# Performance work log

Measured on AMD Instinct MI355X. Metric: run time of the kernel, lower is better.

## Reference

```python
import jax, jax.numpy as jnp
import numpy as np

E, K_TOP, NC = 8, 2, 5
B, L = 64, 512
BN_EPS = 1e-5


def conv1d(x, w, b, pad):
    # x: [B,C,L], w: [O,I,K] (torch OIH layout)
    y = jax.lax.conv_general_dilated(x, w, window_strides=(1,), padding=[(pad, pad)],
                                     dimension_numbers=('NCH', 'OIH', 'NCH'))
    return y + b[None, :, None]


def bn_eval(x, g, b, m, v):
    return g[None, :, None] * (x - m[None, :, None]) * jax.lax.rsqrt(v[None, :, None] + BN_EPS) + b[None, :, None]


def maxpool2(x):
    b, c, l = x.shape
    return x.reshape(b, c, l // 2, 2).max(-1)


def setup_inputs() -> dict:
    key = jax.random.key(0)
    ks = iter(jax.random.split(key, 80))
    nrm = lambda shape, s=0.05: jax.random.normal(next(ks), shape, jnp.float32) * s
    uni = lambda shape: jax.random.uniform(next(ks), shape, jnp.float32) + 0.5
    d = {'x': jax.random.normal(next(ks), (B, 1, L), jnp.float32)}
    d['conv1_w'] = nrm((16, 1, 3)); d['conv1_b'] = nrm((16,))
    # stacked per-expert params: block i has conv w/b + BN gamma/beta/mean/var
    specs = [(64, 16, 3), (128, 64, 9), (256, 128, 11), (512, 256, 25)]
    for i, (co, ci, k) in enumerate(specs, 1):
        d[f'ew{i}'] = nrm((E, co, ci, k)); d[f'eb{i}'] = nrm((E, co))
        d[f'eg{i}'] = uni((E, co)); d[f'ebb{i}'] = nrm((E, co))
        d[f'em{i}'] = nrm((E, co)); d[f'ev{i}'] = uni((E, co))
    d['router_w'] = nrm((E, 16), 0.2); d['router_b'] = nrm((E,))
    d['fc1_w'] = nrm((256, 512)); d['fc1_b'] = nrm((256,))
    d['fc2_w'] = nrm((64, 256)); d['fc2_b'] = nrm((64,))
    d['fc3_w'] = nrm((NC, 64)); d['fc3_b'] = nrm((NC,))
    return d


def _expert(x, e, ew1, eb1, eg1, ebb1, em1, ev1, ew2, eb2, eg2, ebb2, em2, ev2,
            ew3, eb3, eg3, ebb3, em3, ev3, ew4, eb4, eg4, ebb4, em4, ev4):
    # block1: conv3 -> BN -> ReLU -> pool2  (dropout = identity in eval)
    h = maxpool2(jax.nn.relu(bn_eval(conv1d(x, ew1[e], eb1[e], 1), eg1[e], ebb1[e], em1[e], ev1[e])))
    h = maxpool2(jax.nn.relu(bn_eval(conv1d(h, ew2[e], eb2[e], 4), eg2[e], ebb2[e], em2[e], ev2[e])))
    h = maxpool2(jax.nn.relu(bn_eval(conv1d(h, ew3[e], eb3[e], 5), eg3[e], ebb3[e], em3[e], ev3[e])))
    h = maxpool2(jax.nn.relu(bn_eval(conv1d(h, ew4[e], eb4[e], 12), eg4[e], ebb4[e], em4[e], ev4[e])))
    return h  # [B, 512, L//16]


def reference(x, conv1_w, conv1_b,
              ew1, eb1, eg1, ebb1, em1, ev1,
              ew2, eb2, eg2, ebb2, em2, ev2,
              ew3, eb3, eg3, ebb3, em3, ev3,
              ew4, eb4, eg4, ebb4, em4, ev4,
              router_w, router_b, fc1_w, fc1_b, fc2_w, fc2_b, fc3_w, fc3_b):
    b = x.shape[0]
    h = jax.nn.relu(conv1d(x, conv1_w, conv1_b, 1))        # [B,16,L]
    pooled = h.mean(-1)                                    # AdaptiveAvgPool1d(1) -> [B,16]
    logits_r = pooled @ router_w.T + router_b              # [B,E]
    probs = jax.nn.softmax(logits_r, axis=-1)
    gates, idx = jax.lax.top_k(probs, K_TOP)               # [B,k]
    gates = gates / gates.sum(-1, keepdims=True)
    # dense combine weights [B,E]: zero for unselected experts
    w_comb = jnp.zeros((b, E), probs.dtype).at[jnp.arange(b)[:, None], idx].add(gates)
    ep = (ew1, eb1, eg1, ebb1, em1, ev1, ew2, eb2, eg2, ebb2, em2, ev2,
          ew3, eb3, eg3, ebb3, em3, ev3, ew4, eb4, eg4, ebb4, em4, ev4)
    out = jnp.zeros((b, 512, x.shape[2] // 16), x.dtype)
    for e in range(E):  # small fixed expert loop; gate-weighted combine
        out = out + w_comb[:, e, None, None] * _expert(h, e, *ep)
    g = out.mean(-1)                                       # global avg pool -> [B,512]
    g = jax.nn.relu(g @ fc1_w.T + fc1_b)
    g = jax.nn.relu(g @ fc2_w.T + fc2_b)
    cls = g @ fc3_w.T + fc3_b                              # [B,5]
    mp = probs.mean(0)
    cv = jnp.std(mp, ddof=1) / (mp.mean() + 1e-10)         # torch .std() is unbiased
    return cls, cv ** 2
```

## Files before the change

### kernel.cpp

```cpp
#include <hip/hip_runtime.h>
#include <math.h>

#define BN_EPS 1e-5f

typedef _Float16 half8 __attribute__((ext_vector_type(8)));
typedef float floatx16 __attribute__((ext_vector_type(16)));

__global__ __launch_bounds__(256) void conv1_kernel(
    const float* __restrict__ x, const float* __restrict__ w,
    const float* __restrict__ bias, float* __restrict__ h,
    float* __restrict__ pooled) {
  __shared__ float xs[514];
  __shared__ float psum[256];
  const int b = blockIdx.x;
  const int t = threadIdx.x;
  for (int i = t; i < 512; i += 256) xs[i + 1] = x[b * 512 + i];
  if (t == 0) { xs[0] = 0.f; xs[513] = 0.f; }
  __syncthreads();
  const int c  = t >> 4;
  const int l0 = (t & 15) * 32;
  const float w0 = w[c * 3 + 0], w1 = w[c * 3 + 1], w2 = w[c * 3 + 2];
  const float bb = bias[c];
  float s = 0.f;
  float* hrow = h + ((size_t)b * 16 + c) * 512;
  for (int j = 0; j < 32; ++j) {
    const int l = l0 + j;
    float v = fmaf(w0, xs[l], fmaf(w1, xs[l + 1], fmaf(w2, xs[l + 2], bb)));
    v = fmaxf(v, 0.f);
    hrow[l] = v;
    s += v;
  }
  psum[t] = s;
  __syncthreads();
  if ((t & 15) == 0) {
    float tot = 0.f;
    for (int k = 0; k < 16; ++k) tot += psum[t + k];
    pooled[b * 16 + c] = tot * (1.f / 512.f);
  }
}

__global__ void router_kernel(const float* __restrict__ pooled,
                              const float* __restrict__ rw,
                              const float* __restrict__ rb,
                              float* __restrict__ pair_g,
                              int* __restrict__ pair_e,
                              float* __restrict__ out_cv) {
  __shared__ float probs_l[64][8];
  __shared__ float mp[8];
  const int t = threadIdx.x;
  {
    float pl[16];
    for (int c = 0; c < 16; ++c) pl[c] = pooled[t * 16 + c];
    float lg[8];
    float mx = -1e30f;
    for (int e = 0; e < 8; ++e) {
      float a = rb[e];
      for (int c = 0; c < 16; ++c) a = fmaf(pl[c], rw[e * 16 + c], a);
      lg[e] = a;
      mx = fmaxf(mx, a);
    }
    float sum = 0.f;
    for (int e = 0; e < 8; ++e) { lg[e] = expf(lg[e] - mx); sum += lg[e]; }
    const float inv = 1.f / sum;
    for (int e = 0; e < 8; ++e) { lg[e] *= inv; probs_l[t][e] = lg[e]; }
    int e1 = 0; float p1 = lg[0];
    for (int e = 1; e < 8; ++e) if (lg[e] > p1) { p1 = lg[e]; e1 = e; }
    int e2 = -1; float p2 = -1.f;
    for (int e = 0; e < 8; ++e) if (e != e1 && lg[e] > p2) { p2 = lg[e]; e2 = e; }
    const float gs = 1.f / (p1 + p2);
    pair_e[2 * t]     = e1; pair_g[2 * t]     = p1 * gs;
    pair_e[2 * t + 1] = e2; pair_g[2 * t + 1] = p2 * gs;
  }
  __syncthreads();
  if (t < 8) {
    float s = 0.f;
    for (int b = 0; b < 64; ++b) s += probs_l[b][t];
    mp[t] = s * (1.f / 64.f);
  }
  __syncthreads();
  if (t == 0) {
    float mean = 0.f;
    for (int e = 0; e < 8; ++e) mean += mp[e];
    mean *= (1.f / 8.f);
    float var = 0.f;
    for (int e = 0; e < 8; ++e) { const float d = mp[e] - mean; var = fmaf(d, d, var); }
    var *= (1.f / 7.f);
    const float cv = sqrtf(var) / (mean + 1e-10f);
    *out_cv = cv * cv;
  }
}

template <int CI, int K, int KP, int CO>
__global__ __launch_bounds__(256) void repack_kernel(
    const float* __restrict__ ew, _Float16* __restrict__ wrp) {
  constexpr int NCc = CI / 32;
  const int tid = blockIdx.x * 256 + threadIdx.x;
  const int c32 = tid & 31;
  int r = tid >> 5;
  const int co = r % CO; r /= CO;
  const int cic = r % NCc;
  const int e = r / NCc;
  const float* src = ew + ((size_t)(e * CO + co) * CI + cic * 32 + c32) * K;
  float v[K];
#pragma unroll
  for (int dk = 0; dk < K; ++dk) v[dk] = src[dk];
#pragma unroll
  for (int dk = 0; dk < KP; ++dk)
    wrp[(((size_t)(e * NCc + cic) * KP + dk) * CO + co) * 32 + c32] =
        (_Float16)(dk < K ? v[dk] : 0.f);
}

__global__ __launch_bounds__(256) void conv_block1(
    const float* __restrict__ in, const float* __restrict__ ew,
    const float* __restrict__ eb, const float* __restrict__ eg,
    const float* __restrict__ ebb, const float* __restrict__ em,
    const float* __restrict__ ev, const int* __restrict__ pair_e,
    _Float16* __restrict__ out) {
  constexpr int CI = 16, LIN = 512, K = 3, PAD = 1, CO = 64;
  constexpr int W_X  = 66;
  constexpr int W_XP = 68;
  constexpr int WROW = 66;
  __shared__ __align__(16) float xs[CI * W_XP];
  __shared__ __align__(16) float wls[CI * K * WROW];

  const int p  = blockIdx.y;
  const int t  = threadIdx.x;
  const int e  = pair_e[p];
  const int jt = blockIdx.x;
  const float* inp = in + (size_t)(p >> 1) * CI * LIN;
  const int cg = t & 31;
  const int jg = t >> 5;

  float acc0[8], acc1[8];
#pragma unroll
  for (int u = 0; u < 8; ++u) { acc0[u] = 0.f; acc1[u] = 0.f; }
  const int gx0 = jt * 64 - PAD;

  for (int i = t; i < CI * W_XP; i += 256) {
    const int ci = i / W_XP, w = i % W_XP;
    const int gi = gx0 + w;
    float v = 0.f;
    if (w < W_X && gi >= 0 && gi < LIN) v = inp[(size_t)ci * LIN + gi];
    xs[i] = v;
  }
  for (int i = t; i < CI * K * 64; i += 256) {
    const int co = i / (CI * K);
    const int r  = i % (CI * K);
    const int ci = r / K, k = r % K;
    wls[(ci * K + k) * WROW + co] =
        ew[(((size_t)e * CO + co) * CI + ci) * K + k];
  }
  __syncthreads();
  for (int ci = 0; ci < CI; ++ci) {
    const float* xrow = xs + ci * W_XP + jg * 8;
    const float* wrow = wls + ci * K * WROW + 2 * cg;
    float xw[8];
    {
      const float4 a = *(const float4*)(xrow);
      const float4 b = *(const float4*)(xrow + 4);
      xw[0] = a.x; xw[1] = a.y; xw[2] = a.z; xw[3] = a.w;
      xw[4] = b.x; xw[5] = b.y; xw[6] = b.z; xw[7] = b.w;
    }
#pragma unroll
    for (int dk = 0; dk < K; ++dk) {
      const float2 wv = *(const float2*)(wrow + dk * WROW);
#pragma unroll
      for (int u = 0; u < 8; ++u) {
        const float xv = xw[(dk + u) & 7];
        acc0[u] = fmaf(wv.x, xv, acc0[u]);
        acc1[u] = fmaf(wv.y, xv, acc1[u]);
      }
      if (dk + 1 < K) xw[dk & 7] = xrow[dk + 8];
    }
  }

  const int j0 = jt * 32 + jg * 4;
#pragma unroll
  for (int n = 0; n < 2; ++n) {
    const float* acc = n ? acc1 : acc0;
    const int co = 2 * cg + n;
    const int pe = e * CO + co;
    const float s   = eg[pe] * rsqrtf(ev[pe] + BN_EPS);
    const float off = fmaf(eb[pe] - em[pe], s, ebb[pe]);
#pragma unroll
    for (int q = 0; q < 4; ++q) {
      const float y0 = fmaxf(fmaf(acc[2 * q], s, off), 0.f);
      const float y1 = fmaxf(fmaf(acc[2 * q + 1], s, off), 0.f);
      out[((size_t)p * 256 + j0 + q) * CO + co] = (_Float16)fmaxf(y0, y1);
    }
  }
}

template <int CI, int K, int KP, int PAD, int CO, int BM, int LIN, int XN,
          int RING>
__global__ __launch_bounds__(256, 1) void mfma_conv(
    const _Float16* __restrict__ xin, const _Float16* __restrict__ wrp,
    const float* __restrict__ eb, const float* __restrict__ eg,
    const float* __restrict__ ebb, const float* __restrict__ em,
    const float* __restrict__ ev, const int* __restrict__ pair_e,
    _Float16* __restrict__ out) {
  constexpr int NC  = CI / 32;
  constexpr int NPH = NC * KP;
  constexpr int MT  = BM / 128;
  constexpr int NT  = XN / 32;
  constexpr int XWR = XN + KP - 1;
  constexpr int XTN = LIN / XN;
  constexpr int WSL = BM / 4;

  __shared__ __align__(16) _Float16 Bsh[2][XWR * 32];
  __shared__ float sc[BM];
  __shared__ float of[BM];

  const int p  = blockIdx.y;
  const int t  = threadIdx.x;
  const int e  = pair_e[p];
  const int xt = blockIdx.x % XTN;
  const int ct = blockIdx.x / XTN;
  const int cob = ct * BM;
  const int x0  = xt * XN;

  const int lane = t & 63;
  const int wave = t >> 6;
  const int l31 = lane & 31;
  const int lhi = lane >> 5;

  for (int i = t; i < BM; i += 256) {
    const int pe = e * CO + cob + i;
    const float s = eg[pe] * rsqrtf(ev[pe] + BN_EPS);
    sc[i] = s;
    of[i] = fmaf(eb[pe] - em[pe], s, ebb[pe]);
  }

  floatx16 acc[MT][NT];
#pragma unroll
  for (int a = 0; a < MT; ++a)
#pragma unroll
    for (int b = 0; b < NT; ++b)
#pragma unroll
      for (int r = 0; r < 16; ++r) acc[a][b][r] = 0.f;

  const _Float16* xb = xin + (size_t)p * LIN * CI;
  auto stage_B = [&](int cic, int buf) {
    for (int c = t; c < XWR * 4; c += 256) {
      const int row = c >> 2, qq = c & 3;
      const int gx = x0 - PAD + row;
      uint4 v = {0u, 0u, 0u, 0u};
      if (gx >= 0 && gx < LIN)
        v = *(const uint4*)(xb + (size_t)gx * CI + cic * 32 + qq * 8);
      *(uint4*)(&Bsh[buf][row * 32 + qq * 8]) = v;
    }
  };

  const _Float16* Abase = wrp + ((size_t)e * NPH * CO + cob) * 32 +
                          (size_t)(wave * WSL + l31) * 32 + lhi * 8;
  half8 Ar[RING][MT][2];
  auto load_A = [&](int ph, half8 (&dst)[MT][2]) {
    if (ph >= NPH) ph = NPH - 1;
    const _Float16* src = Abase + (size_t)ph * (CO * 32);
#pragma unroll
    for (int mt = 0; mt < MT; ++mt)
#pragma unroll
      for (int ks = 0; ks < 2; ++ks)
        dst[mt][ks] = *(const half8*)(src + mt * 32 * 32 + ks * 16);
  };

  stage_B(0, 0);
#pragma unroll
  for (int d = 0; d < RING; ++d) load_A(d, Ar[d]);
  __syncthreads();
  if (NC > 1) stage_B(1, 1);

  int dk = 0, cic = 0;
  for (int ph0 = 0; ph0 < NPH; ph0 += RING) {
    if (dk == KP) {
      dk = 0; ++cic;
      __syncthreads();
      if (cic + 1 < NC) stage_B(cic + 1, (cic + 1) & 1);
    }
    const _Float16* Bb = &Bsh[cic & 1][0];
#pragma unroll
    for (int d = 0; d < RING; ++d) {
      half8 bf[NT][2];
#pragma unroll
      for (int nt = 0; nt < NT; ++nt)
#pragma unroll
        for (int ks = 0; ks < 2; ++ks)
          bf[nt][ks] = *(const half8*)(Bb + (nt * 32 + l31 + dk) * 32 +
                                       ks * 16 + lhi * 8);
#pragma unroll
      for (int mt = 0; mt < MT; ++mt)
#pragma unroll
        for (int nt = 0; nt < NT; ++nt)
#pragma unroll
          for (int ks = 0; ks < 2; ++ks)
            acc[mt][nt] = __builtin_amdgcn_mfma_f32_32x32x16_f16(
                Ar[d][mt][ks], bf[nt][ks], acc[mt][nt], 0, 0, 0);
      load_A(ph0 + d + RING, Ar[d]);
      ++dk;
    }
  }

#pragma unroll
  for (int mt = 0; mt < MT; ++mt) {
#pragma unroll
    for (int nt = 0; nt < NT; ++nt) {
#pragma unroll
      for (int rq = 0; rq < 4; ++rq) {
        union { _Float16 h[4]; uint2 u; } pk;
#pragma unroll
        for (int j = 0; j < 4; ++j) {
          const int co_l = wave * WSL + mt * 32 + 8 * rq + 4 * lhi + j;
          float y = fmaxf(fmaf(acc[mt][nt][rq * 4 + j], sc[co_l], of[co_l]),
                          0.f);
          const float yp = __shfl_xor(y, 1, 64);
          pk.h[j] = (_Float16)fmaxf(y, yp);
        }
        if ((lane & 1) == 0) {
          const int xp = (x0 + nt * 32 + l31) >> 1;
          const int co = cob + wave * WSL + mt * 32 + 8 * rq + 4 * lhi;
          *(uint2*)(out + ((size_t)p * (LIN / 2) + xp) * CO + co) = pk.u;
        }
      }
    }
  }
}

__global__ __launch_bounds__(256) void combine_kernel(
    const _Float16* __restrict__ out4, const float* __restrict__ pair_g,
    float* __restrict__ g) {
  const int b = blockIdx.x, t = threadIdx.x;
  const float g0 = pair_g[2 * b], g1 = pair_g[2 * b + 1];
  const _Float16* a0 = out4 + (size_t)(2 * b) * 32 * 512;
  const _Float16* a1 = out4 + (size_t)(2 * b + 1) * 32 * 512;
  for (int c = t; c < 512; c += 256) {
    float s0 = 0.f, s1 = 0.f;
    for (int jj = 0; jj < 32; ++jj) {
      s0 += (float)a0[jj * 512 + c];
      s1 += (float)a1[jj * 512 + c];
    }
    g[b * 512 + c] = (g0 * s0 + g1 * s1) * (1.f / 32.f);
  }
}

__global__ __launch_bounds__(256) void head_kernel(
    const float* __restrict__ g, const float* __restrict__ w1,
    const float* __restrict__ b1, const float* __restrict__ w2,
    const float* __restrict__ b2, const float* __restrict__ w3,
    const float* __restrict__ b3, float* __restrict__ out) {
  __shared__ float gl[512];
  __shared__ float h1[256];
  __shared__ float h2[64];
  const int b = blockIdx.x, t = threadIdx.x;
  for (int i = t; i < 512; i += 256) gl[i] = g[b * 512 + i];
  __syncthreads();
  {
    float a = b1[t];
    const float* wr = w1 + (size_t)t * 512;
    for (int k = 0; k < 512; ++k) a = fmaf(gl[k], wr[k], a);
    h1[t] = fmaxf(a, 0.f);
  }
  __syncthreads();
  if (t < 64) {
    float a = b2[t];
    const float* wr = w2 + (size_t)t * 256;
    for (int k = 0; k < 256; ++k) a = fmaf(h1[k], wr[k], a);
    h2[t] = fmaxf(a, 0.f);
  }
  __syncthreads();
  if (t < 5) {
    float a = b3[t];
    const float* wr = w3 + (size_t)t * 64;
    for (int k = 0; k < 64; ++k) a = fmaf(h2[k], wr[k], a);
    out[b * 5 + t] = a;
  }
}

extern "C" void kernel_launch(void* const* d_in, const int* in_sizes, int n_in,
                              void* d_out, int out_size, void* d_ws,
                              size_t ws_size, hipStream_t stream) {
  const float* x   = (const float*)d_in[0];
  const float* c1w = (const float*)d_in[1];
  const float* c1b = (const float*)d_in[2];
  const float* ew1 = (const float*)d_in[3];
  const float* eb1 = (const float*)d_in[4];
  const float* eg1 = (const float*)d_in[5];
  const float* ebb1= (const float*)d_in[6];
  const float* em1 = (const float*)d_in[7];
  const float* ev1 = (const float*)d_in[8];
  const float* ew2 = (const float*)d_in[9];
  const float* eb2 = (const float*)d_in[10];
  const float* eg2 = (const float*)d_in[11];
  const float* ebb2= (const float*)d_in[12];
  const float* em2 = (const float*)d_in[13];
  const float* ev2 = (const float*)d_in[14];
  const float* ew3 = (const float*)d_in[15];
  const float* eb3 = (const float*)d_in[16];
  const float* eg3 = (const float*)d_in[17];
  const float* ebb3= (const float*)d_in[18];
  const float* em3 = (const float*)d_in[19];
  const float* ev3 = (const float*)d_in[20];
  const float* ew4 = (const float*)d_in[21];
  const float* eb4 = (const float*)d_in[22];
  const float* eg4 = (const float*)d_in[23];
  const float* ebb4= (const float*)d_in[24];
  const float* em4 = (const float*)d_in[25];
  const float* ev4 = (const float*)d_in[26];
  const float* rw  = (const float*)d_in[27];
  const float* rb  = (const float*)d_in[28];
  const float* f1w = (const float*)d_in[29];
  const float* f1b = (const float*)d_in[30];
  const float* f2w = (const float*)d_in[31];
  const float* f2b = (const float*)d_in[32];
  const float* f3w = (const float*)d_in[33];
  const float* f3b = (const float*)d_in[34];
  float* out = (float*)d_out;

  float* ws      = (float*)d_ws;
  float* h       = ws;
  float* pooled  = h + 524288;
  float* pair_g  = pooled + 1024;
  int*   pair_e  = (int*)(pair_g + 128);
  _Float16* o1   = (_Float16*)(ws + 525568);
  _Float16* o2   = o1 + 2097152;
  _Float16* o3   = o2 + 2097152;
  _Float16* o4   = o3 + 2097152;
  _Float16* w2r  = o4 + 2097152;
  _Float16* w3r  = w2r + 655360;
  _Float16* w4r  = w3r + 3145728;
  float* g       = (float*)(w4r + 26214400);

  conv1_kernel<<<64, 256, 0, stream>>>(x, c1w, c1b, h, pooled);
  router_kernel<<<1, 64, 0, stream>>>(pooled, rw, rb, pair_g, pair_e, out + 320);

  repack_kernel<64, 9, 10, 128><<<8 * 2 * 128 * 32 / 256, 256, 0, stream>>>(ew2, w2r);
  repack_kernel<128, 11, 12, 256><<<8 * 4 * 256 * 32 / 256, 256, 0, stream>>>(ew3, w3r);
  repack_kernel<256, 25, 25, 512><<<8 * 8 * 512 * 32 / 256, 256, 0, stream>>>(ew4, w4r);

  conv_block1<<<dim3(8, 128), 256, 0, stream>>>(h, ew1, eb1, eg1, ebb1, em1,
                                                ev1, pair_e, o1);
  mfma_conv<64, 9, 10, 4, 128, 128, 256, 128, 5>
      <<<dim3(2, 128), 256, 0, stream>>>(o1, w2r, eb2, eg2, ebb2, em2, ev2,
                                         pair_e, o2);
  mfma_conv<128, 11, 12, 5, 256, 256, 128, 64, 4>
      <<<dim3(2, 128), 256, 0, stream>>>(o2, w3r, eb3, eg3, ebb3, em3, ev3,
                                         pair_e, o3);
  mfma_conv<256, 25, 25, 12, 512, 256, 64, 64, 5>
      <<<dim3(2, 128), 256, 0, stream>>>(o3, w4r, eb4, eg4, ebb4, em4, ev4,
                                         pair_e, o4);

  combine_kernel<<<64, 256, 0, stream>>>(o4, pair_g, g);
  head_kernel<<<64, 256, 0, stream>>>(g, f1w, f1b, f2w, f2b, f3w, f3b, out);
}
```

Before: 387.6 us.

## Add 2D wave tiling, swizzled LDS, and prefetched B fragments in MFMA conv

Wave tiling in the MFMA conv kernel is now generic: waves can split over both output channels (WM) and positions (WN), instead of each wave owning a strip of channels across all positions. The B tile in shared memory is XOR-swizzled per row to reduce bank conflicts. B fragments are double-buffered in registers and loaded one tap ahead. The inner loop now runs over full kernel taps per channel chunk with one barrier per chunk. Block 2's kernel padding drops from 10 taps to 9, removing a wasted all-zero phase. The risk is higher register pressure from the extra bf buffer and a different per-wave A/B reuse balance.

```diff
diff --git a/kernel.cpp b/kernel.cpp
--- a/kernel.cpp
+++ b/kernel.cpp
@@ -191,21 +191,21 @@
   }
 }
 
-template <int CI, int K, int KP, int PAD, int CO, int BM, int LIN, int XN,
-          int RING>
+template <int CI, int K, int KP, int PAD, int CO, int WM, int WN, int MT,
+          int NT, int LIN, int RING>
 __global__ __launch_bounds__(256, 1) void mfma_conv(
     const _Float16* __restrict__ xin, const _Float16* __restrict__ wrp,
     const float* __restrict__ eb, const float* __restrict__ eg,
     const float* __restrict__ ebb, const float* __restrict__ em,
     const float* __restrict__ ev, const int* __restrict__ pair_e,
     _Float16* __restrict__ out) {
+  constexpr int BM  = WM * MT * 32;
+  constexpr int XN  = WN * NT * 32;
   constexpr int NC  = CI / 32;
   constexpr int NPH = NC * KP;
-  constexpr int MT  = BM / 128;
-  constexpr int NT  = XN / 32;
   constexpr int XWR = XN + KP - 1;
   constexpr int XTN = LIN / XN;
-  constexpr int WSL = BM / 4;
+  static_assert(KP % RING == 0, "RING must divide KP");
 
   __shared__ __align__(16) _Float16 Bsh[2][XWR * 32];
   __shared__ float sc[BM];
@@ -221,6 +221,8 @@
 
   const int lane = t & 63;
   const int wave = t >> 6;
+  const int wm = wave / WN;
+  const int wn = wave % WN;
   const int l31 = lane & 31;
   const int lhi = lane >> 5;
 
@@ -247,46 +249,52 @@
       uint4 v = {0u, 0u, 0u, 0u};
       if (gx >= 0 && gx < LIN)
         v = *(const uint4*)(xb + (size_t)gx * CI + cic * 32 + qq * 8);
-      *(uint4*)(&Bsh[buf][row * 32 + qq * 8]) = v;
+      *(uint4*)(&Bsh[buf][row * 32 + (((qq + row) & 3) << 3)]) = v;
     }
   };
 
-  const _Float16* Abase = wrp + ((size_t)e * NPH * CO + cob) * 32 +
-                          (size_t)(wave * WSL + l31) * 32 + lhi * 8;
+  const _Float16* Abase = wrp +
+      (((size_t)e * NPH) * CO + cob + wm * (MT * 32) + l31) * 32 + lhi * 8;
   half8 Ar[RING][MT][2];
-  auto load_A = [&](int ph, half8 (&dst)[MT][2]) {
-    if (ph >= NPH) ph = NPH - 1;
-    const _Float16* src = Abase + (size_t)ph * (CO * 32);
-#pragma unroll
-    for (int mt = 0; mt < MT; ++mt)
-#pragma unroll
-      for (int ks = 0; ks < 2; ++ks)
-        dst[mt][ks] = *(const half8*)(src + mt * 32 * 32 + ks * 16);
-  };
+  half8 bf[2][NT][2];
+
+#define LOAD_A(PH, SLOT)                                                     \
+  do {                                                                       \
+    const int _ph = (PH);                                                    \
+    if (_ph < NPH) {                                                         \
+      const _Float16* _src = Abase + (size_t)_ph * (CO * 32);                \
+      _Pragma("unroll") for (int _mt = 0; _mt < MT; ++_mt)                   \
+          _Pragma("unroll") for (int _ks = 0; _ks < 2; ++_ks)                \
+              Ar[SLOT][_mt][_ks] =                                           \
+          *(const half8*)(_src + _mt * (32 * 32) + _ks * 16);                \
+    }                                                                        \
+  } while (0)
+
+#define LOAD_BF(BI, BB, DK)                                                  \
+  do {                                                                       \
+    const _Float16* _bb = (BB);                                              \
+    const int _dk = (DK);                                                    \
+    _Pragma("unroll") for (int _nt = 0; _nt < NT; ++_nt)                     \
+        _Pragma("unroll") for (int _ks = 0; _ks < 2; ++_ks) {                \
+      const int _row = wn * (NT * 32) + _nt * 32 + l31 + _dk;                \
+      bf[BI][_nt][_ks] = *(const half8*)(                                    \
+          _bb + _row * 32 + ((((_ks << 1) + lhi + _row) & 3) << 3));         \
+    }                                                                        \
+  } while (0)
 
   stage_B(0, 0);
 #pragma unroll
-  for (int d = 0; d < RING; ++d) load_A(d, Ar[d]);
+  for (int d = 0; d < RING; ++d) LOAD_A(d, d);
   __syncthreads();
   if (NC > 1) stage_B(1, 1);
-
-  int dk = 0, cic = 0;
-  for (int ph0 = 0; ph0 < NPH; ph0 += RING) {
-    if (dk == KP) {
-      dk = 0; ++cic;
-      __syncthreads();
-      if (cic + 1 < NC) stage_B(cic + 1, (cic + 1) & 1);
-    }
+  LOAD_BF(0, &Bsh[0][0], 0);
+
+  for (int cic = 0; cic < NC; ++cic) {
     const _Float16* Bb = &Bsh[cic & 1][0];
-#pragma unroll
-    for (int d = 0; d < RING; ++d) {
-      half8 bf[NT][2];
-#pragma unroll
-      for (int nt = 0; nt < NT; ++nt)
-#pragma unroll
-        for (int ks = 0; ks < 2; ++ks)
-          bf[nt][ks] = *(const half8*)(Bb + (nt * 32 + l31 + dk) * 32 +
-                                       ks * 16 + lhi * 8);
+    const int phb = cic * KP;
+#pragma unroll
+    for (int d = 0; d < KP; ++d) {
+      if (d + 1 < KP) LOAD_BF((d + 1) & 1, Bb, d + 1);
 #pragma unroll
       for (int mt = 0; mt < MT; ++mt)
 #pragma unroll
@@ -294,11 +302,15 @@
 #pragma unroll
           for (int ks = 0; ks < 2; ++ks)
             acc[mt][nt] = __builtin_amdgcn_mfma_f32_32x32x16_f16(
-                Ar[d][mt][ks], bf[nt][ks], acc[mt][nt], 0, 0, 0);
-      load_A(ph0 + d + RING, Ar[d]);
-      ++dk;
-    }
-  }
+                Ar[d % RING][mt][ks], bf[d & 1][nt][ks], acc[mt][nt], 0, 0, 0);
+      LOAD_A(phb + d + RING, d % RING);
+    }
+    __syncthreads();
+    if (cic + 2 < NC) stage_B(cic + 2, cic & 1);
+    if (cic + 1 < NC) LOAD_BF(0, &Bsh[(cic + 1) & 1][0], 0);
+  }
+#undef LOAD_A
+#undef LOAD_BF
 
 #pragma unroll
   for (int mt = 0; mt < MT; ++mt) {
@@ -309,15 +321,15 @@
         union { _Float16 h[4]; uint2 u; } pk;
 #pragma unroll
         for (int j = 0; j < 4; ++j) {
-          const int co_l = wave * WSL + mt * 32 + 8 * rq + 4 * lhi + j;
+          const int co_l = wm * (MT * 32) + mt * 32 + 8 * rq + 4 * lhi + j;
           float y = fmaxf(fmaf(acc[mt][nt][rq * 4 + j], sc[co_l], of[co_l]),
                           0.f);
           const float yp = __shfl_xor(y, 1, 64);
           pk.h[j] = (_Float16)fmaxf(y, yp);
         }
         if ((lane & 1) == 0) {
-          const int xp = (x0 + nt * 32 + l31) >> 1;
-          const int co = cob + wave * WSL + mt * 32 + 8 * rq + 4 * lhi;
+          const int xp = (x0 + wn * (NT * 32) + nt * 32 + l31) >> 1;
+          const int co = cob + wm * (MT * 32) + mt * 32 + 8 * rq + 4 * lhi;
           *(uint2*)(out + ((size_t)p * (LIN / 2) + xp) * CO + co) = pk.u;
         }
       }
@@ -425,26 +437,26 @@
   _Float16* o3   = o2 + 2097152;
   _Float16* o4   = o3 + 2097152;
   _Float16* w2r  = o4 + 2097152;
-  _Float16* w3r  = w2r + 655360;
+  _Float16* w3r  = w2r + 589824;
   _Float16* w4r  = w3r + 3145728;
   float* g       = (float*)(w4r + 26214400);
 
   conv1_kernel<<<64, 256, 0, stream>>>(x, c1w, c1b, h, pooled);
   router_kernel<<<1, 64, 0, stream>>>(pooled, rw, rb, pair_g, pair_e, out + 320);
 
-  repack_kernel<64, 9, 10, 128><<<8 * 2 * 128 * 32 / 256, 256, 0, stream>>>(ew2, w2r);
+  repack_kernel<64, 9, 9, 128><<<8 * 2 * 128 * 32 / 256, 256, 0, stream>>>(ew2, w2r);
   repack_kernel<128, 11, 12, 256><<<8 * 4 * 256 * 32 / 256, 256, 0, stream>>>(ew3, w3r);
   repack_kernel<256, 25, 25, 512><<<8 * 8 * 512 * 32 / 256, 256, 0, stream>>>(ew4, w4r);
 
   conv_block1<<<dim3(8, 128), 256, 0, stream>>>(h, ew1, eb1, eg1, ebb1, em1,
                                                 ev1, pair_e, o1);
-  mfma_conv<64, 9, 10, 4, 128, 128, 256, 128, 5>
+  mfma_conv<64, 9, 9, 4, 128, 2, 2, 2, 2, 256, 3>
       <<<dim3(2, 128), 256, 0, stream>>>(o1, w2r, eb2, eg2, ebb2, em2, ev2,
                                          pair_e, o2);
-  mfma_conv<128, 11, 12, 5, 256, 256, 128, 64, 4>
+  mfma_conv<128, 11, 12, 5, 256, 4, 1, 2, 2, 128, 3>
       <<<dim3(2, 128), 256, 0, stream>>>(o2, w3r, eb3, eg3, ebb3, em3, ev3,
                                          pair_e, o3);
-  mfma_conv<256, 25, 25, 12, 512, 256, 64, 64, 5>
+  mfma_conv<256, 25, 25, 12, 512, 4, 1, 2, 2, 64, 5>
       <<<dim3(2, 128), 256, 0, stream>>>(o3, w4r, eb4, eg4, ebb4, em4, ev4,
                                          pair_e, o4);
 
```

Measured after the change: 449.1 us. 15.9% more time.
